# Performance work log

Hardware: AMD Instinct MI355X
Metric: run time of the kernel (lower is better)

## Reference

```python
import jax, jax.numpy as jnp
import numpy as np
import math

D_MODEL = 1024
D_STATE = 128
D_CONV = 4
EXPAND = 2
HEADDIM = 64
NGROUPS = 1
CHUNK = 256
D_INNER = EXPAND * D_MODEL
D_SSM = D_INNER
NHEADS = D_SSM // HEADDIM
CONV_DIM = D_SSM + 2 * NGROUPS * D_STATE
D_IN_PROJ = 2 * D_INNER + 2 * NGROUPS * D_STATE + NHEADS
BATCH = 2
SEQLEN = 4096
EPS = 1e-5


def segsum(x):
    # x: (..., T) -> (..., T, T); segsum[i, j] = sum_{j < k <= i} x[k], -inf above diagonal
    T = x.shape[-1]
    xc = jnp.cumsum(x, axis=-1)
    d = xc[..., :, None] - xc[..., None, :]
    mask = jnp.tril(jnp.ones((T, T), dtype=bool))
    return jnp.where(mask, d, -jnp.inf)


def setup_inputs() -> dict:
    key = jax.random.key(0)
    ks = jax.random.split(key, 8)
    u = jax.random.normal(ks[0], (BATCH, SEQLEN, D_MODEL), jnp.float32)
    W_in = jax.random.normal(ks[1], (D_IN_PROJ, D_MODEL), jnp.float32) / np.sqrt(D_MODEL)
    conv_w = jax.random.uniform(ks[2], (CONV_DIM, D_CONV), jnp.float32, -1.0, 1.0) / np.sqrt(D_CONV)
    conv_b = jnp.zeros((CONV_DIM,), jnp.float32)
    # dt_bias init as in the torch module: inverse-softplus of dt ~ LogUniform(1e-3, 1e-1)
    dt = jnp.exp(jax.random.uniform(ks[3], (NHEADS,), jnp.float32) * (math.log(0.1) - math.log(0.001)) + math.log(0.001))
    dt = jnp.maximum(dt, 1e-4)
    dt_bias = dt + jnp.log(-jnp.expm1(-dt))
    A_log = jnp.log(jax.random.uniform(ks[4], (NHEADS,), jnp.float32, 1.0, 16.0))
    D = jnp.ones((NHEADS,), jnp.float32)
    norm_w = jnp.ones((D_SSM,), jnp.float32)
    W_out = jax.random.normal(ks[5], (D_MODEL, D_INNER), jnp.float32) / np.sqrt(D_INNER)
    return {"u": u, "W_in": W_in, "conv_w": conv_w, "conv_b": conv_b,
            "dt_bias": dt_bias, "A_log": A_log, "D": D, "norm_w": norm_w, "W_out": W_out}


def reference(u, W_in, conv_w, conv_b, dt_bias, A_log, D, norm_w, W_out):
    b, L, _ = u.shape
    zxbcdt = u @ W_in.T  # (b, L, d_in_proj); d_mlp == 0 for this config
    z, xBC, dt = jnp.split(zxbcdt, [D_SSM, D_SSM + CONV_DIM], axis=-1)

    # depthwise causal conv1d + SiLU (kernel width D_CONV, left padding)
    xpad = jnp.pad(xBC, ((0, 0), (D_CONV - 1, 0), (0, 0)))
    acc = conv_b
    for k in range(D_CONV):
        acc = acc + xpad[:, k:k + L, :] * conv_w[:, k]
    xBC = jax.nn.silu(acc)

    x, Bm, Cm = jnp.split(xBC, [D_SSM, D_SSM + NGROUPS * D_STATE], axis=-1)
    hpg = NHEADS // NGROUPS  # heads per B/C group
    Bh = jnp.repeat(Bm.reshape(b, L, NGROUPS, D_STATE), hpg, axis=2)  # (b, L, h, n)
    Ch = jnp.repeat(Cm.reshape(b, L, NGROUPS, D_STATE), hpg, axis=2)
    x = x.reshape(b, L, NHEADS, HEADDIM)

    dt = jax.nn.softplus(dt + dt_bias)  # (b, L, h)
    A = -jnp.exp(A_log)  # (h,)

    # ---- SSD chunked selective scan ----
    nc = L // CHUNK
    xc = x.reshape(b, nc, CHUNK, NHEADS, HEADDIM)
    Bc = Bh.reshape(b, nc, CHUNK, NHEADS, D_STATE)
    Cc = Ch.reshape(b, nc, CHUNK, NHEADS, D_STATE)
    dt_bclh = dt.reshape(b, nc, CHUNK, NHEADS)
    dA = jnp.transpose(dt_bclh, (0, 3, 1, 2)) * A[None, :, None, None]  # (b, h, c, l)
    A_cs = jnp.cumsum(dA, axis=-1)  # (b, h, c, l)

    # intra-chunk (diagonal block) outputs
    Ldiag = jnp.exp(segsum(dA))  # (b, h, c, l, s)
    x_dt = xc * dt_bclh[..., None]  # fold dt into x
    Y_diag = jnp.einsum('bclhn,bcshn,bhcls,bcshp->bclhp', Cc, Bc, Ldiag, x_dt)

    # per-chunk final states
    decay_states = jnp.exp(A_cs[..., -1:] - A_cs)  # (b, h, c, l)
    states = jnp.einsum('bclhn,bhcl,bclhp->bchpn', Bc, decay_states, x_dt)

    # inter-chunk recurrence via segsum over chunk-level decays
    chunk_sum = jnp.pad(A_cs[..., -1], ((0, 0), (0, 0), (1, 0)))  # (b, h, c+1)
    decay_chunk = jnp.exp(segsum(chunk_sum))  # (b, h, c+1, c+1)
    states = jnp.concatenate([jnp.zeros_like(states[:, :1]), states], axis=1)
    new_states = jnp.einsum('bhzc,bchpn->bzhpn', decay_chunk, states)
    prev_states = new_states[:, :-1]  # state entering each chunk

    # state -> output contribution
    Y_off = jnp.einsum('bclhn,bchpn,bhcl->bclhp', Cc, prev_states, jnp.exp(A_cs))

    y = (Y_diag + Y_off).reshape(b, L, NHEADS, HEADDIM) + x * D[None, None, :, None]
    y = y.reshape(b, L, D_SSM)

    # gated RMSNorm (norm_before_gate=False, ngroups=1 -> full-dim norm)
    y = y * jax.nn.silu(z)
    y = y * jax.lax.rsqrt(jnp.mean(jnp.square(y), axis=-1, keepdims=True) + EPS) * norm_w
    return y @ W_out.T
```

## Files before the change

kernel.cpp:

```cpp
#include <hip/hip_runtime.h>
#include <hip/hip_bf16.h>

#define ZX_LD   4384
#define XC_LD   2304
#define NH      32
#define HD      64
#define DS      128
#define CHK     256
#define NC      16
#define LTOT    4096
#define ROWS    8192
#define DSSM    2048
#define YPAD    80

typedef __bf16 bf16_t;
typedef bf16_t bf16x8 __attribute__((ext_vector_type(8)));
typedef float  f32x4  __attribute__((ext_vector_type(4)));
typedef unsigned short u16x8 __attribute__((ext_vector_type(8)));

__device__ inline float bf2f(unsigned short u) {
  unsigned int x = ((unsigned int)u) << 16;
  float f; __builtin_memcpy(&f, &x, 4); return f;
}

#define GLOAD_LDS16(gp, lp) \
  __builtin_amdgcn_global_load_lds((const __attribute__((address_space(1))) void*)(gp), \
                                   (__attribute__((address_space(3))) void*)(lp), 16, 0, 0)

__global__ __launch_bounds__(256) void cast_f32_bf16(
    const float* __restrict__ in, bf16_t* __restrict__ out,
    long nvalid, long total)
{
  const long e0 = ((long)blockIdx.x * 256 + threadIdx.x) * 8;
  if (e0 >= total) return;
  bf16x8 o;
  if (e0 + 8 <= nvalid) {
    const float4 a = *(const float4*)(in + e0);
    const float4 b = *(const float4*)(in + e0 + 4);
    o[0]=(bf16_t)a.x; o[1]=(bf16_t)a.y; o[2]=(bf16_t)a.z; o[3]=(bf16_t)a.w;
    o[4]=(bf16_t)b.x; o[5]=(bf16_t)b.y; o[6]=(bf16_t)b.z; o[7]=(bf16_t)b.w;
  } else {
#pragma unroll
    for (int j = 0; j < 8; ++j) o[j] = (bf16_t)0.f;
  }
  *(bf16x8*)(out + e0) = o;
}

template<bool BF16OUT>
__global__ __launch_bounds__(256) void gemm_bt_mfma(
    const bf16_t* __restrict__ A, const bf16_t* __restrict__ B,
    void* __restrict__ Cv, int M, int N, int K,
    int lda, int ldb, int ldc)
{
  __shared__ __align__(16) bf16_t As[128 * 32];
  __shared__ __align__(16) bf16_t Bs[128 * 32];
  const int tid  = threadIdx.x;
  const int lane = tid & 63;
  const int wave = tid >> 6;

  const int nwg  = gridDim.x * gridDim.y;
  int wgid = blockIdx.y * gridDim.x + blockIdx.x;
  {
    const int xcd = wgid & 7, local = wgid >> 3;
    const int q = nwg >> 3, r = nwg & 7;
    wgid = (xcd < r ? xcd * (q + 1) : r * (q + 1) + (xcd - r) * q) + local;
  }
  const int bm = (wgid / gridDim.x) * 128;
  const int bn = (wgid % gridDim.x) * 128;

  const int wr = (wave >> 1) * 64;
  const int wc = (wave & 1) * 64;

  const int c0   = wave * 2;
  const int lrow = lane >> 2;
  const int lcol = (lane & 3) * 8;
  const bf16_t* Ag0 = A + (size_t)(bm + c0 * 16 + lrow) * lda + lcol;
  const bf16_t* Ag1 = A + (size_t)(bm + c0 * 16 + 16 + lrow) * lda + lcol;
  const bf16_t* Bg0 = B + (size_t)(bn + c0 * 16 + lrow) * ldb + lcol;
  const bf16_t* Bg1 = B + (size_t)(bn + c0 * 16 + 16 + lrow) * ldb + lcol;
  bf16_t* Al0 = As + c0 * 512;
  bf16_t* Al1 = As + c0 * 512 + 512;
  bf16_t* Bl0 = Bs + c0 * 512;
  bf16_t* Bl1 = Bs + c0 * 512 + 512;

  f32x4 acc[4][4];
#pragma unroll
  for (int i = 0; i < 4; ++i)
#pragma unroll
    for (int j = 0; j < 4; ++j) acc[i][j] = (f32x4){0.f, 0.f, 0.f, 0.f};

  const int nk = K >> 5;
  for (int kt = 0; kt < nk; ++kt) {
    const int k0 = kt * 32;
    __syncthreads();
    GLOAD_LDS16(Ag0 + k0, Al0);
    GLOAD_LDS16(Ag1 + k0, Al1);
    GLOAD_LDS16(Bg0 + k0, Bl0);
    GLOAD_LDS16(Bg1 + k0, Bl1);
    __syncthreads();

    const bf16_t* Ab = As + (wr + (lane & 15)) * 32 + (lane >> 4) * 8;
    const bf16_t* Bb = Bs + (wc + (lane & 15)) * 32 + (lane >> 4) * 8;
    bf16x8 af[4], bfv[4];
#pragma unroll
    for (int mi = 0; mi < 4; ++mi) af[mi]  = *(const bf16x8*)(Ab + mi * 512);
#pragma unroll
    for (int ni = 0; ni < 4; ++ni) bfv[ni] = *(const bf16x8*)(Bb + ni * 512);
#pragma unroll
    for (int mi = 0; mi < 4; ++mi)
#pragma unroll
      for (int ni = 0; ni < 4; ++ni)
        acc[mi][ni] = __builtin_amdgcn_mfma_f32_16x16x32_bf16(af[mi], bfv[ni], acc[mi][ni], 0, 0, 0);
  }

  const int crow0 = bm + wr + (lane >> 4) * 4;
  const int ccol0 = bn + wc + (lane & 15);
#pragma unroll
  for (int ni = 0; ni < 4; ++ni) {
    const int ccol = ccol0 + ni * 16;
    if (ccol < N) {
#pragma unroll
      for (int mi = 0; mi < 4; ++mi) {
#pragma unroll
        for (int j = 0; j < 4; ++j) {
          if constexpr (BF16OUT) {
            ((bf16_t*)Cv)[(size_t)(crow0 + mi * 16 + j) * ldc + ccol] = (bf16_t)acc[mi][ni][j];
          } else {
            ((float*)Cv)[(size_t)(crow0 + mi * 16 + j) * ldc + ccol] = acc[mi][ni][j];
          }
        }
      }
    }
  }
}

__global__ __launch_bounds__(256) void conv_silu_kernel(
    const bf16_t* __restrict__ zx, const float* __restrict__ cw,
    const float* __restrict__ cb, bf16_t* __restrict__ xconv)
{
  const int ch  = blockIdx.x * 256 + threadIdx.x;
  const int row = blockIdx.y;
  const int l   = row & (LTOT - 1);
  float acc = cb[ch];
#pragma unroll
  for (int k = 0; k < 4; ++k) {
    const int ls = l - 3 + k;
    if (ls >= 0)
      acc = fmaf((float)zx[(size_t)(row - 3 + k) * ZX_LD + 2048 + ch], cw[ch*4 + k], acc);
  }
  const float r = acc / (1.f + __expf(-acc));
  xconv[(size_t)row * XC_LD + ch] = (bf16_t)r;
}

__global__ __launch_bounds__(256) void dt_kernel(
    const bf16_t* __restrict__ zx, const float* __restrict__ dtb,
    float* __restrict__ dtv)
{
  const int idx = blockIdx.x * 256 + threadIdx.x;
  const int row = idx >> 5;
  const int hh  = idx & 31;
  const float x = (float)zx[(size_t)row * ZX_LD + 4352 + hh] + dtb[hh];
  dtv[idx] = (x > 20.f) ? x : log1pf(__expf(x));
}

__global__ __launch_bounds__(256) void chunk_states_kernel(
    const float* __restrict__ dtv, const float* __restrict__ A_log,
    const bf16_t* __restrict__ xconv,
    float* __restrict__ acs, float* __restrict__ totals,
    float* __restrict__ states)
{
  const int bid = blockIdx.x;
  const int h = bid & 31;
  const int c = (bid >> 5) & 15;
  const int b = bid >> 9;
  const int rowbase = b * LTOT + c * CHK;
  const int tid = threadIdx.x;
  const int lane = tid & 63;
  const int wv   = tid >> 6;
  const int ln15 = lane & 15;
  const int lg   = lane >> 4;

  __shared__ float sWdt[256];
  __shared__ float wsum[4];
  __shared__ __align__(16) bf16_t xT[64 * 64];
  __shared__ __align__(16) bf16_t Bt[128 * 64];
  unsigned short* Btu = (unsigned short*)Bt;

  const float dt = dtv[(size_t)(rowbase + tid) * NH + h];
  const float Ah = -__expf(A_log[h]);
  float v = dt * Ah;
#pragma unroll
  for (int off = 1; off < 64; off <<= 1) {
    float up = __shfl_up(v, off, 64);
    if ((tid & 63) >= off) v += up;
  }
  if ((tid & 63) == 63) wsum[tid >> 6] = v;
  __syncthreads();
  const float w0 = wsum[0], w1 = wsum[1], w2 = wsum[2], w3 = wsum[3];
  float base = 0.f;
  if (wv > 0) base += w0;
  if (wv > 1) base += w1;
  if (wv > 2) base += w2;
  const float acsl  = v + base;
  const float total = w0 + w1 + w2 + w3;
  acs[bid * 256 + tid] = acsl;
  if (tid == 0) totals[(b * 32 + h) * 16 + c] = total;
  sWdt[tid] = __expf(total - acsl) * dt;

  f32x4 acc[4][2];
#pragma unroll
  for (int i = 0; i < 4; ++i)
#pragma unroll
    for (int j = 0; j < 2; ++j) acc[i][j] = (f32x4){0.f, 0.f, 0.f, 0.f};

  const int s  = tid >> 2;
  const int p0 = (tid & 3) * 16;
  const int n0 = (tid & 3) * 32;

  for (int ls = 0; ls < 4; ++ls) {
    const int l0 = ls * 64;
    __syncthreads();
    {
      const float wgt = sWdt[l0 + s];
      const bf16_t* xr = xconv + (size_t)(rowbase + l0 + s) * XC_LD + h * HD + p0;
      u16x8 v0 = *(const u16x8*)xr;
      u16x8 v1 = *(const u16x8*)(xr + 8);
#pragma unroll
      for (int j = 0; j < 8; ++j) {
        const int p = p0 + j;
        xT[p * 64 + ((((s >> 3) ^ (p & 7)) << 3) | (s & 7))] = (bf16_t)(bf2f(v0[j]) * wgt);
      }
#pragma unroll
      for (int j = 0; j < 8; ++j) {
        const int p = p0 + 8 + j;
        xT[p * 64 + ((((s >> 3) ^ (p & 7)) << 3) | (s & 7))] = (bf16_t)(bf2f(v1[j]) * wgt);
      }
      const bf16_t* br = xconv + (size_t)(rowbase + l0 + s) * XC_LD + 2048 + n0;
#pragma unroll
      for (int q = 0; q < 4; ++q) {
        u16x8 t = *(const u16x8*)(br + q * 8);
#pragma unroll
        for (int j = 0; j < 8; ++j) {
          const int n = n0 + q * 8 + j;
          Btu[n * 64 + ((((s >> 3) ^ (n & 7)) << 3) | (s & 7))] = t[j];
        }
      }
    }
    __syncthreads();
#pragma unroll
    for (int ks = 0; ks < 2; ++ks) {
      bf16x8 af[4];
#pragma unroll
      for (int mi = 0; mi < 4; ++mi) {
        const int row = mi * 16 + ln15;
        const int chunk = (ks * 4 + lg) ^ (row & 7);
        af[mi] = *(const bf16x8*)(xT + row * 64 + chunk * 8);
      }
#pragma unroll
      for (int ni = 0; ni < 2; ++ni) {
        const int nrow = wv * 32 + ni * 16 + ln15;
        const int chunk = (ks * 4 + lg) ^ (nrow & 7);
        bf16x8 bfr = *(const bf16x8*)(Bt + nrow * 64 + chunk * 8);
#pragma unroll
        for (int mi = 0; mi < 4; ++mi)
          acc[mi][ni] = __builtin_amdgcn_mfma_f32_16x16x32_bf16(af[mi], bfr, acc[mi][ni], 0, 0, 0);
      }
    }
  }

  const size_t sbase = (size_t)bid * (HD * DS);
#pragma unroll
  for (int mi = 0; mi < 4; ++mi) {
#pragma unroll
    for (int ni = 0; ni < 2; ++ni) {
      const int n = wv * 32 + ni * 16 + ln15;
#pragma unroll
      for (int j = 0; j < 4; ++j) {
        const int p = mi * 16 + lg * 4 + j;
        states[sbase + p * DS + n] = acc[mi][ni][j];
      }
    }
  }
}

__global__ __launch_bounds__(256) void chunk_prefix_kernel(
    const float* __restrict__ st, const float* __restrict__ totals,
    bf16_t* __restrict__ prevbf)
{
  const int bh = blockIdx.x;
  const int b = bh >> 5;
  const int h = bh & 31;
  const int e = blockIdx.y;
  const int tid = threadIdx.x;
  float P = 0.f;
  for (int c = 0; c < NC; ++c) {
    const size_t idx = (size_t)((b * 16 + c) * 32 + h) * (HD * DS) + e * 256 + tid;
    const float g = __expf(totals[bh * 16 + c]);
    prevbf[idx] = (bf16_t)P;
    P = fmaf(P, g, st[idx]);
  }
}

__global__ __launch_bounds__(256) void y_kernel_mfma(
    const bf16_t* __restrict__ xconv, const float* __restrict__ dtv,
    const float* __restrict__ acs,   const bf16_t* __restrict__ prevbf,
    const float* __restrict__ Dv,    bf16_t* __restrict__ ypre, int ypld)
{
  const int bid = blockIdx.x;
  const int lt = bid & 3;
  const int h  = (bid >> 2) & 31;
  const int c  = (bid >> 7) & 15;
  const int b  = bid >> 11;
  const int bch = (b * 16 + c) * 32 + h;
  const int rowbase = b * LTOT + c * CHK;
  const int tid  = threadIdx.x;
  const int lane = tid & 63;
  const int wv   = tid >> 6;
  const int ln15 = lane & 15;
  const int lg   = lane >> 4;

  __shared__ float sAcs[256];
  __shared__ float sDt[256];
  __shared__ __align__(16) bf16_t Sl[64 * YPAD];
  __shared__ __align__(16) bf16_t xT[64 * YPAD];
  unsigned short* xTu = (unsigned short*)xT;

  sAcs[tid] = acs[bch * 256 + tid];
  sDt[tid]  = dtv[(size_t)(rowbase + tid) * NH + h];
  __syncthreads();

  bf16x8 cf[4][4];
#pragma unroll
  for (int mi = 0; mi < 4; ++mi) {
    const bf16_t* crow = xconv + (size_t)(rowbase + lt*64 + mi*16 + ln15) * XC_LD + 2176 + lg * 8;
#pragma unroll
    for (int ks = 0; ks < 4; ++ks) cf[mi][ks] = *(const bf16x8*)(crow + ks * 32);
  }

  f32x4 acc[4];
#pragma unroll
  for (int mi = 0; mi < 4; ++mi) acc[mi] = (f32x4){0.f, 0.f, 0.f, 0.f};
  {
    const bf16_t* pb = prevbf + ((size_t)bch * 64 + 16 * wv + ln15) * 128 + lg * 8;
#pragma unroll
    for (int ks = 0; ks < 4; ++ks) {
      bf16x8 pf = *(const bf16x8*)(pb + ks * 32);
#pragma unroll
      for (int mi = 0; mi < 4; ++mi)
        acc[mi] = __builtin_amdgcn_mfma_f32_16x16x32_bf16(cf[mi][ks], pf, acc[mi], 0, 0, 0);
    }
  }
#pragma unroll
  for (int mi = 0; mi < 4; ++mi) {
#pragma unroll
    for (int j = 0; j < 4; ++j)
      acc[mi][j] *= __expf(sAcs[lt*64 + mi*16 + lg*4 + j]);
  }

  for (int st = 0; st <= lt; ++st) {
    __syncthreads();
    {
      const int s  = tid >> 2;
      const int p0 = (tid & 3) * 16;
      const bf16_t* xr = xconv + (size_t)(rowbase + st*64 + s) * XC_LD + h * HD + p0;
      u16x8 v0 = *(const u16x8*)xr;
      u16x8 v1 = *(const u16x8*)(xr + 8);
#pragma unroll
      for (int j = 0; j < 8; ++j) xTu[(p0 + j) * YPAD + s] = v0[j];
#pragma unroll
      for (int j = 0; j < 8; ++j) xTu[(p0 + 8 + j) * YPAD + s] = v1[j];
    }

    f32x4 sa[4];
#pragma unroll
    for (int mi = 0; mi < 4; ++mi) sa[mi] = (f32x4){0.f, 0.f, 0.f, 0.f};
    {
      const bf16_t* brow = xconv + (size_t)(rowbase + st*64 + 16*wv + ln15) * XC_LD + 2048 + lg * 8;
#pragma unroll
      for (int ks = 0; ks < 4; ++ks) {
        bf16x8 bfr = *(const bf16x8*)(brow + ks * 32);
#pragma unroll
        for (int mi = 0; mi < 4; ++mi)
          sa[mi] = __builtin_amdgcn_mfma_f32_16x16x32_bf16(cf[mi][ks], bfr, sa[mi], 0, 0, 0);
      }
    }
    {
      const int sg = st * 64 + 16 * wv + ln15;
      const float as  = sAcs[sg];
      const float dts = sDt[sg];
#pragma unroll
      for (int mi = 0; mi < 4; ++mi) {
#pragma unroll
        for (int j = 0; j < 4; ++j) {
          const int lloc = mi * 16 + lg * 4 + j;
          const int ll = lt * 64 + lloc;
          float wvv = 0.f;
          if (ll >= sg) wvv = sa[mi][j] * __expf(sAcs[ll] - as) * dts;
          Sl[lloc * YPAD + 16 * wv + ln15] = (bf16_t)wvv;
        }
      }
    }
    __syncthreads();

#pragma unroll
    for (int ks2 = 0; ks2 < 2; ++ks2) {
      bf16x8 xf = *(const bf16x8*)(xT + (16 * wv + ln15) * YPAD + ks2 * 32 + lg * 8);
#pragma unroll
      for (int mi = 0; mi < 4; ++mi) {
        bf16x8 sf = *(const bf16x8*)(Sl + (mi * 16 + ln15) * YPAD + ks2 * 32 + lg * 8);
        acc[mi] = __builtin_amdgcn_mfma_f32_16x16x32_bf16(sf, xf, acc[mi], 0, 0, 0);
      }
    }
  }

  const float Dh = Dv[h];
  const int p = 16 * wv + ln15;
#pragma unroll
  for (int mi = 0; mi < 4; ++mi) {
#pragma unroll
    for (int j = 0; j < 4; ++j) {
      const int lloc = mi * 16 + lg * 4 + j;
      const int row  = rowbase + lt * 64 + lloc;
      const float xv = (float)xT[p * YPAD + lloc];
      ypre[(size_t)row * ypld + h * HD + p] = (bf16_t)(acc[mi][j] + xv * Dh);
    }
  }
}

__global__ __launch_bounds__(256) void rmsnorm_gate_kernel(
    const bf16_t* __restrict__ zx, const float* __restrict__ normw,
    bf16_t* __restrict__ ypre_bf)
{
  const int row = blockIdx.x;
  const int tid = threadIdx.x;
  const unsigned short* zr = (const unsigned short*)(zx + (size_t)row * ZX_LD);
  u16x8 yv = *(const u16x8*)(zr + 2048 + tid * 8);
  u16x8 zv = *(const u16x8*)(zr + tid * 8);
  float vals[8];
  float ss = 0.f;
#pragma unroll
  for (int j = 0; j < 8; ++j) {
    const float y = bf2f(yv[j]);
    const float z = bf2f(zv[j]);
    const float sz = z / (1.f + __expf(-z));
    const float v = y * sz;
    vals[j] = v;
    ss += v * v;
  }
#pragma unroll
  for (int off = 32; off >= 1; off >>= 1) ss += __shfl_xor(ss, off, 64);
  __shared__ float red[4];
  if ((tid & 63) == 0) red[tid >> 6] = ss;
  __syncthreads();
  const float tot = red[0] + red[1] + red[2] + red[3];
  const float scale = rsqrtf(tot / (float)DSSM + 1e-5f);
  const float4 w0 = *(const float4*)(normw + tid * 8);
  const float4 w1 = *(const float4*)(normw + tid * 8 + 4);
  bf16x8 o;
  o[0] = (bf16_t)(vals[0] * scale * w0.x);
  o[1] = (bf16_t)(vals[1] * scale * w0.y);
  o[2] = (bf16_t)(vals[2] * scale * w0.z);
  o[3] = (bf16_t)(vals[3] * scale * w0.w);
  o[4] = (bf16_t)(vals[4] * scale * w1.x);
  o[5] = (bf16_t)(vals[5] * scale * w1.y);
  o[6] = (bf16_t)(vals[6] * scale * w1.z);
  o[7] = (bf16_t)(vals[7] * scale * w1.w);
  *(bf16x8*)(ypre_bf + (size_t)row * DSSM + tid * 8) = o;
}

extern "C" void kernel_launch(void* const* d_in, const int* in_sizes, int n_in,
                              void* d_out, int out_size, void* d_ws, size_t ws_size,
                              hipStream_t stream)
{
  const float* u       = (const float*)d_in[0];
  const float* W_in    = (const float*)d_in[1];
  const float* conv_w  = (const float*)d_in[2];
  const float* conv_b  = (const float*)d_in[3];
  const float* dt_bias = (const float*)d_in[4];
  const float* A_log   = (const float*)d_in[5];
  const float* Dv      = (const float*)d_in[6];
  const float* norm_w  = (const float*)d_in[7];
  const float* W_out   = (const float*)d_in[8];
  float* out = (float*)d_out;

  const size_t OFF_XC  = (size_t)ROWS * ZX_LD * 2;
  const size_t OFF_DT  = OFF_XC  + (size_t)ROWS * XC_LD * 2;
  const size_t OFF_ACS = OFF_DT  + (size_t)ROWS * NH * 4;
  const size_t OFF_TOT = OFF_ACS + (size_t)1024 * 256 * 4;
  const size_t OFF_ST  = OFF_TOT + 4096;
  const size_t OFF_AR  = OFF_ST  + (size_t)1024 * HD * DS * 4;
  const size_t need    = OFF_AR  + (size_t)ROWS * XC_LD * 2;
  if (ws_size < need) return;

  char* w = (char*)d_ws;
  bf16_t* zxb     = (bf16_t*)w;
  bf16_t* xconv   = (bf16_t*)(w + OFF_XC);
  float*  dtv     = (float*)(w + OFF_DT);
  float*  acsb    = (float*)(w + OFF_ACS);
  float*  totals  = (float*)(w + OFF_TOT);
  float*  states  = (float*)(w + OFF_ST);
  bf16_t* arena   = (bf16_t*)(w + OFF_AR);
  bf16_t* u_bf    = arena;
  bf16_t* Wpad    = arena + (size_t)ROWS * 1024;
  bf16_t* prevbf  = arena;
  bf16_t* ypre_bf = arena;
  bf16_t* Wout_bf = arena + (size_t)ROWS * DSSM;
  bf16_t* ypre_ov = zxb + 2048;

  {
    const long n_u = (long)ROWS * 1024;
    cast_f32_bf16<<<dim3((n_u/8 + 255)/256), 256, 0, stream>>>(u, u_bf, n_u, n_u);
    const long n_wv = (long)4384 * 1024, n_wt = (long)4480 * 1024;
    cast_f32_bf16<<<dim3((n_wt/8 + 255)/256), 256, 0, stream>>>(W_in, Wpad, n_wv, n_wt);
    const long n_wo = (long)1024 * DSSM;
    cast_f32_bf16<<<dim3((n_wo/8 + 255)/256), 256, 0, stream>>>(W_out, Wout_bf, n_wo, n_wo);
  }
  gemm_bt_mfma<true><<<dim3(35, 64), 256, 0, stream>>>(u_bf, Wpad, zxb, ROWS, 4384, 1024,
                                                       1024, 1024, ZX_LD);
  conv_silu_kernel<<<dim3(9, ROWS), 256, 0, stream>>>(zxb, conv_w, conv_b, xconv);
  dt_kernel<<<dim3((ROWS * NH) / 256), 256, 0, stream>>>(zxb, dt_bias, dtv);
  chunk_states_kernel<<<dim3(1024), 256, 0, stream>>>(dtv, A_log, xconv, acsb, totals, states);
  chunk_prefix_kernel<<<dim3(64, 32), 256, 0, stream>>>(states, totals, prevbf);
  y_kernel_mfma<<<dim3(4096), 256, 0, stream>>>(xconv, dtv, acsb, prevbf, Dv, ypre_ov, ZX_LD);
  rmsnorm_gate_kernel<<<dim3(ROWS), 256, 0, stream>>>(zxb, norm_w, ypre_bf);
  gemm_bt_mfma<false><<<dim3(8, 64), 256, 0, stream>>>(ypre_bf, Wout_bf, out, ROWS, 1024, 2048,
                                                       2048, 2048, 1024);
}
```

Baseline: 508.3 us.

## Remap block order in chunk kernels and prefetch next x/B tiles in y kernel

Block indices in chunk_states_kernel and y_kernel_mfma are permuted so that consecutive hardware block IDs are spread across batch/chunk/head groups, which is meant to balance work and cache use across XCDs. In y_kernel_mfma, the x and B fragments for the next sub-tile are loaded from global memory into registers before the current tile's score computation, so load latency overlaps with MFMA work. The cost is more live registers, which may lower occupancy.

```diff
diff --git a/kernel.cpp b/kernel.cpp
--- a/kernel.cpp
+++ b/kernel.cpp
@@ -169,7 +169,8 @@
     float* __restrict__ acs, float* __restrict__ totals,
     float* __restrict__ states)
 {
-  const int bid = blockIdx.x;
+  const int bid0 = blockIdx.x;
+  const int bid  = (bid0 & 7) * 128 + (bid0 >> 3);
   const int h = bid & 31;
   const int c = (bid >> 5) & 15;
   const int b = bid >> 9;
@@ -306,7 +307,8 @@
     const float* __restrict__ acs,   const bf16_t* __restrict__ prevbf,
     const float* __restrict__ Dv,    bf16_t* __restrict__ ypre, int ypld)
 {
-  const int bid = blockIdx.x;
+  const int bid0 = blockIdx.x;
+  const int bid  = (bid0 & 7) * 512 + (bid0 >> 3);
   const int lt = bid & 3;
   const int h  = (bid >> 2) & 31;
   const int c  = (bid >> 7) & 15;
@@ -357,33 +359,47 @@
       acc[mi][j] *= __expf(sAcs[lt*64 + mi*16 + lg*4 + j]);
   }
 
+  u16x8 xv0, xv1;
+  bf16x8 bfp[4];
+  {
+    const bf16_t* xr = xconv + (size_t)(rowbase + (tid >> 2)) * XC_LD + h * HD + (tid & 3) * 16;
+    xv0 = *(const u16x8*)xr;
+    xv1 = *(const u16x8*)(xr + 8);
+    const bf16_t* brow = xconv + (size_t)(rowbase + 16*wv + ln15) * XC_LD + 2048 + lg * 8;
+#pragma unroll
+    for (int ks = 0; ks < 4; ++ks) bfp[ks] = *(const bf16x8*)(brow + ks * 32);
+  }
+
   for (int st = 0; st <= lt; ++st) {
     __syncthreads();
     {
       const int s  = tid >> 2;
       const int p0 = (tid & 3) * 16;
-      const bf16_t* xr = xconv + (size_t)(rowbase + st*64 + s) * XC_LD + h * HD + p0;
-      u16x8 v0 = *(const u16x8*)xr;
-      u16x8 v1 = *(const u16x8*)(xr + 8);
-#pragma unroll
-      for (int j = 0; j < 8; ++j) xTu[(p0 + j) * YPAD + s] = v0[j];
-#pragma unroll
-      for (int j = 0; j < 8; ++j) xTu[(p0 + 8 + j) * YPAD + s] = v1[j];
+#pragma unroll
+      for (int j = 0; j < 8; ++j) xTu[(p0 + j) * YPAD + s] = xv0[j];
+#pragma unroll
+      for (int j = 0; j < 8; ++j) xTu[(p0 + 8 + j) * YPAD + s] = xv1[j];
     }
 
     f32x4 sa[4];
 #pragma unroll
     for (int mi = 0; mi < 4; ++mi) sa[mi] = (f32x4){0.f, 0.f, 0.f, 0.f};
-    {
-      const bf16_t* brow = xconv + (size_t)(rowbase + st*64 + 16*wv + ln15) * XC_LD + 2048 + lg * 8;
-#pragma unroll
-      for (int ks = 0; ks < 4; ++ks) {
-        bf16x8 bfr = *(const bf16x8*)(brow + ks * 32);
-#pragma unroll
-        for (int mi = 0; mi < 4; ++mi)
-          sa[mi] = __builtin_amdgcn_mfma_f32_16x16x32_bf16(cf[mi][ks], bfr, sa[mi], 0, 0, 0);
-      }
-    }
+#pragma unroll
+    for (int ks = 0; ks < 4; ++ks) {
+#pragma unroll
+      for (int mi = 0; mi < 4; ++mi)
+        sa[mi] = __builtin_amdgcn_mfma_f32_16x16x32_bf16(cf[mi][ks], bfp[ks], sa[mi], 0, 0, 0);
+    }
+
+    if (st < lt) {
+      const bf16_t* xr = xconv + (size_t)(rowbase + (st+1)*64 + (tid >> 2)) * XC_LD + h * HD + (tid & 3) * 16;
+      xv0 = *(const u16x8*)xr;
+      xv1 = *(const u16x8*)(xr + 8);
+      const bf16_t* brow = xconv + (size_t)(rowbase + (st+1)*64 + 16*wv + ln15) * XC_LD + 2048 + lg * 8;
+#pragma unroll
+      for (int ks = 0; ks < 4; ++ks) bfp[ks] = *(const bf16x8*)(brow + ks * 32);
+    }
+
     {
       const int sg = st * 64 + 16 * wv + ln15;
       const float as  = sAcs[sg];
```

Result: no change. 502.7 us (-1.1%).
